# Kernel tuning notes

Hardware: AMD Instinct MI355X
Metric: run time of the kernel (lower is better)

## Reference

```python
import jax, jax.numpy as jnp
import numpy as np

EMBED = 3072
NQ = 32
NKV = 8
HD = EMBED // NQ  # 96
GROUPS = NQ // NKV  # 4
ROPE_BASE = 10000.0


def apply_rope(t, positions):
    # t: [b, h, s, d]; positions: [s] int
    d = t.shape[-1]
    inv_freq = 1.0 / (ROPE_BASE ** (jnp.arange(0, d, 2, dtype=jnp.float32) / d))  # [d/2]
    ang = positions.astype(jnp.float32)[:, None] * inv_freq[None, :]  # [s, d/2]
    cos = jnp.cos(ang)[None, None]  # [1,1,s,d/2]
    sin = jnp.sin(ang)[None, None]
    t1, t2 = t[..., : d // 2], t[..., d // 2 :]
    return jnp.concatenate([t1 * cos - t2 * sin, t2 * cos + t1 * sin], axis=-1)


def setup_inputs() -> dict:
    key = jax.random.key(0)
    k1, k2, k3 = jax.random.split(key, 3)
    b, s = 2, 2048
    x = jax.random.normal(k1, (b, s, EMBED), dtype=jnp.float32)
    positions = jnp.arange(s, dtype=jnp.int32)
    mask = jnp.triu(jnp.ones((s, s), dtype=bool), k=1)  # True = masked (causal)
    qkv_size = NQ * HD + 2 * NKV * HD  # 4608
    W_qkv = jax.random.normal(k2, (qkv_size, EMBED), dtype=jnp.float32) * (EMBED ** -0.5)
    W_o = jax.random.normal(k3, (EMBED, EMBED), dtype=jnp.float32) * (EMBED ** -0.5)
    return {"x": x, "positions": positions, "mask": mask, "W_qkv": W_qkv, "W_o": W_o}


def reference(x, positions, mask, W_qkv, W_o):
    b, s, _ = x.shape
    scaling = HD ** -0.5
    qkv = x @ W_qkv.T  # [b, s, 4608]
    q_size, kv_size = NQ * HD, NKV * HD
    q = qkv[..., :q_size].reshape(b, s, NQ, HD).transpose(0, 2, 1, 3)          # [b,NQ,s,d]
    k = qkv[..., q_size : q_size + kv_size].reshape(b, s, NKV, HD).transpose(0, 2, 1, 3)
    v = qkv[..., q_size + kv_size :].reshape(b, s, NKV, HD).transpose(0, 2, 1, 3)
    q = apply_rope(q, positions)
    k = apply_rope(k, positions)
    q = q.reshape(b, NKV, GROUPS, s, HD)
    scores = jnp.einsum("bkgsd,bktd->bkgst", q, k) * scaling  # [b,NKV,G,s,s]
    scores = jnp.where(mask[None, None, None], -jnp.inf, scores)
    attn = jax.nn.softmax(scores, axis=-1)
    out = jnp.einsum("bkgst,bktd->bkgsd", attn, v)
    out = out.reshape(b, NQ, s, HD).transpose(0, 2, 1, 3).reshape(b, s, NQ * HD)
    return out @ W_o.T
```

## Files before the change

### kernel.cpp

```cpp
#include <hip/hip_runtime.h>
#include <cstdint>

typedef unsigned short u16;
typedef unsigned int u32;
typedef __attribute__((ext_vector_type(4))) float f32x4;
typedef __attribute__((ext_vector_type(8))) __bf16 bf16x8;
typedef __attribute__((ext_vector_type(8))) unsigned short u16x8;
typedef __attribute__((ext_vector_type(4))) unsigned int u32x4;

#define S_LEN 2048
#define BATCH 2
#define NQH 32
#define NKVH 8
#define HD 96
#define EMB 3072
#define QKVN 4608
#define KOFF 3072
#define VOFF 3840
#define KSP 104

__device__ __forceinline__ u16 f2b(float f) {
    u32 u = __float_as_uint(f);
    u32 r = (u + 0x7fffu + ((u >> 16) & 1u)) >> 16;
    return (u16)r;
}
__device__ __forceinline__ float b2f(u16 h) { return __uint_as_float(((u32)h) << 16); }
__device__ __forceinline__ u32 cvtpk(float lo, float hi) {
    u32 r;
    asm("v_cvt_pk_bf16_f32 %0, %1, %2" : "=v"(r) : "v"(lo), "v"(hi));
    return r;
}

__global__ __launch_bounds__(256) void conv_f2b(const float* __restrict__ in,
                                                u16* __restrict__ outp, int n8) {
    const int i = blockIdx.x * 256 + threadIdx.x;
    if (i >= n8) return;
    const f32x4* q = (const f32x4*)(in + (size_t)i * 8);
    const f32x4 a = q[0], b = q[1];
    u16x8 t;
#pragma unroll
    for (int j = 0; j < 4; ++j) {
        t[j] = f2b(a[j]);
        t[j + 4] = f2b(b[j]);
    }
    *(u16x8*)(outp + (size_t)i * 8) = t;
}

typedef __attribute__((address_space(1))) const uint32_t gas_u32;
typedef __attribute__((address_space(3))) uint32_t las_u32;
__device__ __forceinline__ void gld_lds16(const u16* g, u16* l) {
    __builtin_amdgcn_global_load_lds((gas_u32*)g, (las_u32*)l, 16, 0, 0);
}

#define WAITV8 asm volatile("s_waitcnt vmcnt(8)" ::: "memory")
#define LGKM0 asm volatile("s_waitcnt lgkmcnt(0)" ::: "memory")
#define BARRIERM asm volatile("s_barrier" ::: "memory")
#define SCHEDB __builtin_amdgcn_sched_barrier(0)

__device__ __forceinline__ void stage32(const u16* __restrict__ G, int ldg, int k0,
                                        u16* buf, int tid) {
#pragma unroll
    for (int L = 0; L < 2; ++L) {
        const int c = L * 512 + tid;
        const int r = c >> 2;
        const int sg = (c & 3) ^ ((r >> 1) & 3);
        const u16* src = G + (size_t)r * ldg + k0 + sg * 8;
        u16* dst = buf + (L * 512 + (tid & 448)) * 8;
        gld_lds16(src, dst);
    }
}

__device__ __forceinline__ bf16x8 frag32(const u16* buf, int row, int s) {
    const int sg = s ^ ((row >> 1) & 3);
    return *(const bf16x8*)(buf + row * 32 + sg * 8);
}

template <bool OUTF32>
__global__ __launch_bounds__(512, 1) void gemm_bt32(const u16* __restrict__ Ap,
                                                    const u16* __restrict__ Bp,
                                                    void* __restrict__ Cp,
                                                    int M, int N, int K, int ldc) {
    __shared__ __align__(16) u16 S[65536];
    const int tid = threadIdx.x;
    const int lane = tid & 63;
    const int lrow = lane & 15, lhi = lane >> 4;
    const int wid = tid >> 6;
    const int wr = wid >> 2, wc = wid & 3;
    const int bm = blockIdx.y * 256, bn = blockIdx.x * 256;
    const u16* Ab = Ap + (size_t)bm * K;
    const u16* Bb = Bp + (size_t)bn * K;

    f32x4 acc[8][4] = {};
    const int nt = K >> 5;
    const int arow0 = wr * 128 + lrow;
    const int brow0 = wc * 64 + lrow;

#pragma unroll
    for (int t = 0; t < 3; ++t) {
        stage32(Ab, K, t * 32, S + t * 16384, tid);
        stage32(Bb, K, t * 32, S + t * 16384 + 8192, tid);
    }

    for (int t = 0; t < nt; ++t) {
        const u16* Ac = S + (t & 3) * 16384;
        const u16* Bc = Ac + 8192;
        u16* Sn = S + ((t + 3) & 3) * 16384;
        const int kn = (t + 3 < nt) ? (t + 3) * 32 : 0;

        WAITV8;
        BARRIERM;

        bf16x8 af[8], bfr[2];
#pragma unroll
        for (int mi = 0; mi < 8; ++mi) af[mi] = frag32(Ac, arow0 + mi * 16, lhi);
#pragma unroll
        for (int ni = 0; ni < 2; ++ni) bfr[ni] = frag32(Bc, brow0 + ni * 16, lhi);
        stage32(Ab, K, kn, Sn, tid);
        LGKM0;
        SCHEDB;
        __builtin_amdgcn_s_setprio(1);
#pragma unroll
        for (int mi = 0; mi < 8; ++mi)
#pragma unroll
            for (int ni = 0; ni < 2; ++ni)
                acc[mi][ni] = __builtin_amdgcn_mfma_f32_16x16x32_bf16(af[mi], bfr[ni],
                                                                      acc[mi][ni], 0, 0, 0);
        __builtin_amdgcn_s_setprio(0);

#pragma unroll
        for (int ni = 0; ni < 2; ++ni) bfr[ni] = frag32(Bc, brow0 + (ni + 2) * 16, lhi);
        stage32(Bb, K, kn, Sn + 8192, tid);
        LGKM0;
        SCHEDB;
        __builtin_amdgcn_s_setprio(1);
#pragma unroll
        for (int mi = 0; mi < 8; ++mi)
#pragma unroll
            for (int ni = 0; ni < 2; ++ni)
                acc[mi][ni + 2] = __builtin_amdgcn_mfma_f32_16x16x32_bf16(af[mi], bfr[ni],
                                                                          acc[mi][ni + 2], 0, 0, 0);
        __builtin_amdgcn_s_setprio(0);
    }

    const int orow = bm + wr * 128 + lhi * 4;
    const int ocol = bn + wc * 64 + lrow;
#pragma unroll
    for (int mi = 0; mi < 8; ++mi)
#pragma unroll
        for (int ni = 0; ni < 4; ++ni)
#pragma unroll
            for (int r = 0; r < 4; ++r) {
                const size_t idx = (size_t)(orow + mi * 16 + r) * ldc + ocol + ni * 16;
                if constexpr (OUTF32)
                    ((float*)Cp)[idx] = acc[mi][ni][r];
                else
                    ((u16*)Cp)[idx] = f2b(acc[mi][ni][r]);
            }
}

__global__ __launch_bounds__(256) void gqa_rope8(u16* __restrict__ qkv,
                                                 const int* __restrict__ positions) {
    const int i = blockIdx.x * 256 + threadIdx.x;
    const int pc = i % 6;
    int t = i / 6;
    const int head = t % (NQH + NKVH);
    const int bs = t / (NQH + NKVH);
    const int pos = positions[bs & (S_LEN - 1)];
    const size_t base = (size_t)bs * QKVN +
                        (head < NQH ? head * HD : KOFF + (head - NQH) * HD) + pc * 8;
    const u16x8 a = *(const u16x8*)(qkv + base);
    const u16x8 b = *(const u16x8*)(qkv + base + 48);
    u16x8 ra, rb;
#pragma unroll
    for (int jj = 0; jj < 8; ++jj) {
        const int pair = pc * 8 + jj;
        const float invf = __expf(-(float)(2 * pair) * (1.0f / 96.0f) * 9.210340371976184f);
        const float ang = (float)pos * invf;
        float sn, cs;
        __sincosf(ang, &sn, &cs);
        const float t1 = b2f(a[jj]), t2 = b2f(b[jj]);
        ra[jj] = f2b(t1 * cs - t2 * sn);
        rb[jj] = f2b(t2 * cs + t1 * sn);
    }
    *(u16x8*)(qkv + base) = ra;
    *(u16x8*)(qkv + base + 48) = rb;
}

__global__ __launch_bounds__(256) void gqa_attn5(const u16* __restrict__ qkv,
                                                 u16* __restrict__ out) {
    __shared__ __align__(16) u16 Ks[64 * KSP];
    __shared__ __align__(16) u16 Vtmp[64 * 96];
    __shared__ __align__(16) u16 Vt[96 * 72];

    const int tid = threadIdx.x;
    const int wave = tid >> 6, lane = tid & 63;
    const int lrow = lane & 15, lhi = lane >> 4;
    const int bx = blockIdx.x;
    const int qt32 = 63 - (bx >> 4);
    const int kvh = (bx >> 1) & 7, bb = bx & 1;
    const int qh = kvh * 4 + wave;
    const int srow0 = bb * S_LEN + qt32 * 32;
    const int kb_last = (qt32 * 32 + 31) >> 6;
    const float cl2 = 0.10206207261596575f * 1.4426950408889634f;

    bf16x8 bq[2][3];
#pragma unroll
    for (int qt = 0; qt < 2; ++qt)
#pragma unroll
        for (int kd = 0; kd < 3; ++kd)
            bq[qt][kd] = *(const bf16x8*)(qkv + (size_t)(srow0 + qt * 16 + lrow) * QKVN +
                                          qh * 96 + kd * 32 + lhi * 8);

    float m_s[2] = {-3e38f, -3e38f}, l_s[2] = {0.0f, 0.0f};
    f32x4 oacc[6][2] = {};

    const int s0 = lrow + ((lane & 16) ? 32 : 0);
    const int s1 = s0 + 16;
    const bool khi = (lane & 32) != 0;

    const size_t kvrow0 = (size_t)(bb * S_LEN) * QKVN;
    u16x8 kreg[3], vreg[3];

    {
        const size_t kbase = kvrow0 + KOFF + (size_t)kvh * 96;
        const size_t vbase = kvrow0 + VOFF + (size_t)kvh * 96;
#pragma unroll
        for (int i = 0; i < 3; ++i) {
            const int u = tid + 256 * i;
            const int so = (u % 12) * 8, sr = u / 12;
            kreg[i] = *(const u16x8*)(qkv + kbase + (size_t)sr * QKVN + so);
            vreg[i] = *(const u16x8*)(qkv + vbase + (size_t)sr * QKVN + so);
        }
#pragma unroll
        for (int i = 0; i < 3; ++i) {
            const int u = tid + 256 * i;
            const int so = (u % 12) * 8, sr = u / 12;
            *(u16x8*)(Ks + sr * KSP + so) = kreg[i];
            *(u16x8*)(Vtmp + sr * 96 + so) = vreg[i];
        }
        __syncthreads();
#pragma unroll
        for (int i = 0; i < 3; ++i) {
            const int u = tid + 256 * i;
            const int td = u % 96, ts8 = u / 96;
            u16x8 c;
#pragma unroll
            for (int j = 0; j < 8; ++j) c[j] = Vtmp[(ts8 * 8 + j) * 96 + td];
            *(u16x8*)(Vt + td * 72 + ts8 * 8) = c;
        }
    }

    for (int kb = 0; kb <= kb_last; ++kb) {
        if (kb < kb_last) {
            const size_t kbase2 = kvrow0 + (size_t)((kb + 1) * 64) * QKVN + KOFF + kvh * 96;
            const size_t vbase2 = kvrow0 + (size_t)((kb + 1) * 64) * QKVN + VOFF + kvh * 96;
#pragma unroll
            for (int i = 0; i < 3; ++i) {
                const int u = tid + 256 * i;
                const int so = (u % 12) * 8, sr = u / 12;
                kreg[i] = *(const u16x8*)(qkv + kbase2 + (size_t)sr * QKVN + so);
                vreg[i] = *(const u16x8*)(qkv + vbase2 + (size_t)sr * QKVN + so);
            }
        }
        __syncthreads();

        bf16x8 ka[4][3];
#pragma unroll
        for (int kt = 0; kt < 4; ++kt)
#pragma unroll
            for (int kd = 0; kd < 3; ++kd)
                ka[kt][kd] = *(const bf16x8*)(Ks + (kt * 16 + lrow) * KSP + kd * 32 + lhi * 8);

        const int qoff = qt32 * 32 - kb * 64;
        const bool lastkb = (kb == kb_last);
        u32 bp[2][2][4];

#pragma unroll
        for (int qt = 0; qt < 2; ++qt) {
            const int qrelmax = qoff + qt * 16 + 15;
            f32x4 sacc[4] = {};
#pragma unroll
            for (int kt = 0; kt < 4; ++kt) {
                if (lastkb && kt * 16 > qrelmax) continue;
#pragma unroll
                for (int kd = 0; kd < 3; ++kd)
                    sacc[kt] = __builtin_amdgcn_mfma_f32_16x16x32_bf16(ka[kt][kd], bq[qt][kd],
                                                                       sacc[kt], 0, 0, 0);
            }
            float p[4][4];
            float mx = -3e38f;
            if (lastkb) {
                const int qrel = qoff + qt * 16 + lrow;
#pragma unroll
                for (int kt = 0; kt < 4; ++kt)
#pragma unroll
                    for (int r = 0; r < 4; ++r) {
                        const bool live = (kt * 16 + lhi * 4 + r) <= qrel;
                        const float s = live ? sacc[kt][r] : -3e38f;
                        p[kt][r] = s;
                        mx = fmaxf(mx, s);
                    }
            } else {
#pragma unroll
                for (int kt = 0; kt < 4; ++kt)
#pragma unroll
                    for (int r = 0; r < 4; ++r) {
                        p[kt][r] = sacc[kt][r];
                        mx = fmaxf(mx, sacc[kt][r]);
                    }
            }
            mx = fmaxf(mx, __shfl_xor(mx, 16));
            mx = fmaxf(mx, __shfl_xor(mx, 32));
            float mn = m_s[qt];
            if (!__all(mx - mn <= 20.0f)) {
                const float mnew = fmaxf(mn, mx);
                const float alpha = exp2f((mn - mnew) * cl2);
                m_s[qt] = mnew;
                mn = mnew;
                l_s[qt] *= alpha;
#pragma unroll
                for (int dt = 0; dt < 6; ++dt)
#pragma unroll
                    for (int r = 0; r < 4; ++r) oacc[dt][qt][r] *= alpha;
            }
            float rs = 0.0f;
#pragma unroll
            for (int kt = 0; kt < 4; ++kt)
#pragma unroll
                for (int r = 0; r < 4; ++r) {
                    const float pv = exp2f((p[kt][r] - mn) * cl2);
                    p[kt][r] = pv;
                    rs += pv;
                }
            rs += __shfl_xor(rs, 16);
            rs += __shfl_xor(rs, 32);
            l_s[qt] += rs;
            u32 pk[4][2];
#pragma unroll
            for (int kt = 0; kt < 4; ++kt) {
                pk[kt][0] = cvtpk(p[kt][0], p[kt][1]);
                pk[kt][1] = cvtpk(p[kt][2], p[kt][3]);
            }
#pragma unroll
            for (int kk = 0; kk < 2; ++kk) {
                const u32 a0 = (u32)__shfl((int)pk[kk * 2][0], s0, 64);
                const u32 b0 = (u32)__shfl((int)pk[kk * 2 + 1][0], s0, 64);
                const u32 a1 = (u32)__shfl((int)pk[kk * 2][1], s0, 64);
                const u32 b1 = (u32)__shfl((int)pk[kk * 2 + 1][1], s0, 64);
                const u32 a2 = (u32)__shfl((int)pk[kk * 2][0], s1, 64);
                const u32 b2 = (u32)__shfl((int)pk[kk * 2 + 1][0], s1, 64);
                const u32 a3 = (u32)__shfl((int)pk[kk * 2][1], s1, 64);
                const u32 b3 = (u32)__shfl((int)pk[kk * 2 + 1][1], s1, 64);
                bp[qt][kk][0] = khi ? b0 : a0;
                bp[qt][kk][1] = khi ? b1 : a1;
                bp[qt][kk][2] = khi ? b2 : a2;
                bp[qt][kk][3] = khi ? b3 : a3;
            }
        }

#pragma unroll
        for (int dt = 0; dt < 6; ++dt) {
            bf16x8 va[2];
#pragma unroll
            for (int kk = 0; kk < 2; ++kk)
                va[kk] = *(const bf16x8*)(Vt + (dt * 16 + lrow) * 72 + kk * 32 + lhi * 8);
#pragma unroll
            for (int qt = 0; qt < 2; ++qt)
#pragma unroll
                for (int kk = 0; kk < 2; ++kk) {
                    const u32x4 bv = {bp[qt][kk][0], bp[qt][kk][1], bp[qt][kk][2], bp[qt][kk][3]};
                    oacc[dt][qt] = __builtin_amdgcn_mfma_f32_16x16x32_bf16(
                        va[kk], __builtin_bit_cast(bf16x8, bv), oacc[dt][qt], 0, 0, 0);
                }
        }

        __syncthreads();
        if (kb < kb_last) {
#pragma unroll
            for (int i = 0; i < 3; ++i) {
                const int u = tid + 256 * i;
                const int so = (u % 12) * 8, sr = u / 12;
                *(u16x8*)(Ks + sr * KSP + so) = kreg[i];
                *(u16x8*)(Vtmp + sr * 96 + so) = vreg[i];
            }
            __syncthreads();
#pragma unroll
            for (int i = 0; i < 3; ++i) {
                const int u = tid + 256 * i;
                const int td = u % 96, ts8 = u / 96;
                u16x8 c;
#pragma unroll
                for (int j = 0; j < 8; ++j) c[j] = Vtmp[(ts8 * 8 + j) * 96 + td];
                *(u16x8*)(Vt + td * 72 + ts8 * 8) = c;
            }
        }
    }

    const size_t obase = (size_t)srow0 * EMB + qh * 96;
#pragma unroll
    for (int qt = 0; qt < 2; ++qt) {
        const float inv = 1.0f / l_s[qt];
        const size_t rbase = obase + (size_t)(qt * 16 + lrow) * EMB;
#pragma unroll
        for (int dt = 0; dt < 6; ++dt)
#pragma unroll
            for (int rp = 0; rp < 2; ++rp) {
                const u32 pair = cvtpk(oacc[dt][qt][2 * rp] * inv, oacc[dt][qt][2 * rp + 1] * inv);
                *(u32*)(out + rbase + dt * 16 + lhi * 4 + 2 * rp) = pair;
            }
    }
}

extern "C" void kernel_launch(void* const* d_in, const int* in_sizes, int n_in,
                              void* d_out, int out_size, void* d_ws, size_t ws_size,
                              hipStream_t stream) {
    const float* x = (const float*)d_in[0];
    const int* positions = (const int*)d_in[1];
    const float* W_qkv = (const float*)d_in[3];
    const float* W_o = (const float*)d_in[4];
    float* out = (float*)d_out;

    const int M = BATCH * S_LEN;
    const size_t QKV_E = (size_t)M * QKVN;
    const size_t X_E = (size_t)M * EMB;
    const size_t WQKV_E = (size_t)QKVN * EMB;
    const size_t WO_E = (size_t)EMB * EMB;

    u16* qkv = (u16*)d_ws;
    u16* scratch = qkv + QKV_E;
    u16* xb = scratch;
    u16* wqkvb = (u16*)d_out;
    u16* wob = (u16*)d_ws;

    conv_f2b<<<(int)(X_E / 8 / 256), 256, 0, stream>>>(x, xb, (int)(X_E / 8));
    conv_f2b<<<(int)(WQKV_E / 8 / 256), 256, 0, stream>>>(W_qkv, wqkvb, (int)(WQKV_E / 8));
    gemm_bt32<false>
        <<<dim3(QKVN / 256, M / 256), 512, 0, stream>>>(xb, wqkvb, qkv, M, QKVN, EMB, QKVN);
    gqa_rope8<<<(BATCH * S_LEN * (NQH + NKVH) * 6) / 256, 256, 0, stream>>>(qkv, positions);
    gqa_attn5<<<dim3(1024), 256, 0, stream>>>(qkv, scratch);
    conv_f2b<<<(int)(WO_E / 8 / 256), 256, 0, stream>>>(W_o, wob, (int)(WO_E / 8));
    gemm_bt32<true>
        <<<dim3(EMB / 256, M / 256), 512, 0, stream>>>(scratch, wob, out, M, EMB, EMB, EMB);
}
```

Before: 597.3 us.

## Split longest causal attention tiles across two blocks with merge kernel

The 512 query tiles with the most keys (the last quarter of rows per batch) are now split into two blocks. Each block processes half of the key range and writes unnormalized fp32 partial outputs plus its max and sum into d_out as scratch. A new merge kernel combines the two halves with log-sum-exp rescaling and writes bf16. This is meant to reduce tail imbalance in the causal attention grid, at the cost of an extra launch and fp32 partial traffic.

```diff
diff --git a/kernel.cpp b/kernel.cpp
--- a/kernel.cpp
+++ b/kernel.cpp
@@ -18,6 +18,7 @@
 #define KOFF 3072
 #define VOFF 3840
 #define KSP 104
+#define CL2 0.14724601498759837f
 
 __device__ __forceinline__ u16 f2b(float f) {
     u32 u = __float_as_uint(f);
@@ -186,8 +187,9 @@
     *(u16x8*)(qkv + base + 48) = rb;
 }
 
-__global__ __launch_bounds__(256) void gqa_attn5(const u16* __restrict__ qkv,
-                                                 u16* __restrict__ out) {
+__global__ __launch_bounds__(256) void gqa_attn6(const u16* __restrict__ qkv,
+                                                 u16* __restrict__ out,
+                                                 float* __restrict__ part) {
     __shared__ __align__(16) u16 Ks[64 * KSP];
     __shared__ __align__(16) u16 Vtmp[64 * 96];
     __shared__ __align__(16) u16 Vt[96 * 72];
@@ -196,12 +198,33 @@
     const int wave = tid >> 6, lane = tid & 63;
     const int lrow = lane & 15, lhi = lane >> 4;
     const int bx = blockIdx.x;
-    const int qt32 = 63 - (bx >> 4);
-    const int kvh = (bx >> 1) & 7, bb = bx & 1;
+
+    int qt32, kvh, bb, sp, kb_lo, kb_hi;
+    bool dosplit;
+    if (bx < 768) {
+        qt32 = 47 - (bx >> 4);
+        kvh = (bx >> 1) & 7;
+        bb = bx & 1;
+        sp = 0;
+        kb_lo = 0;
+        kb_hi = (qt32 * 32 + 31) >> 6;
+        dosplit = false;
+    } else {
+        const int s = bx - 768;
+        qt32 = 63 - (s >> 5);
+        const int r = s & 31;
+        kvh = (r >> 2) & 7;
+        bb = (r >> 1) & 1;
+        sp = r & 1;
+        const int kb_last = (qt32 * 32 + 31) >> 6;
+        const int half = (kb_last + 1) >> 1;
+        kb_lo = sp ? half : 0;
+        kb_hi = sp ? kb_last : half - 1;
+        dosplit = true;
+    }
+    const int kb_abs_last = (qt32 * 32 + 31) >> 6;
     const int qh = kvh * 4 + wave;
     const int srow0 = bb * S_LEN + qt32 * 32;
-    const int kb_last = (qt32 * 32 + 31) >> 6;
-    const float cl2 = 0.10206207261596575f * 1.4426950408889634f;
 
     bf16x8 bq[2][3];
 #pragma unroll
@@ -222,8 +245,8 @@
     u16x8 kreg[3], vreg[3];
 
     {
-        const size_t kbase = kvrow0 + KOFF + (size_t)kvh * 96;
-        const size_t vbase = kvrow0 + VOFF + (size_t)kvh * 96;
+        const size_t kbase = kvrow0 + (size_t)(kb_lo * 64) * QKVN + KOFF + (size_t)kvh * 96;
+        const size_t vbase = kvrow0 + (size_t)(kb_lo * 64) * QKVN + VOFF + (size_t)kvh * 96;
 #pragma unroll
         for (int i = 0; i < 3; ++i) {
             const int u = tid + 256 * i;
@@ -250,8 +273,8 @@
         }
     }
 
-    for (int kb = 0; kb <= kb_last; ++kb) {
-        if (kb < kb_last) {
+    for (int kb = kb_lo; kb <= kb_hi; ++kb) {
+        if (kb < kb_hi) {
             const size_t kbase2 = kvrow0 + (size_t)((kb + 1) * 64) * QKVN + KOFF + kvh * 96;
             const size_t vbase2 = kvrow0 + (size_t)((kb + 1) * 64) * QKVN + VOFF + kvh * 96;
 #pragma unroll
@@ -272,7 +295,7 @@
                 ka[kt][kd] = *(const bf16x8*)(Ks + (kt * 16 + lrow) * KSP + kd * 32 + lhi * 8);
 
         const int qoff = qt32 * 32 - kb * 64;
-        const bool lastkb = (kb == kb_last);
+        const bool lastkb = (kb == kb_abs_last);
         u32 bp[2][2][4];
 
 #pragma unroll
@@ -314,7 +337,7 @@
             float mn = m_s[qt];
             if (!__all(mx - mn <= 20.0f)) {
                 const float mnew = fmaxf(mn, mx);
-                const float alpha = exp2f((mn - mnew) * cl2);
+                const float alpha = exp2f((mn - mnew) * CL2);
                 m_s[qt] = mnew;
                 mn = mnew;
                 l_s[qt] *= alpha;
@@ -328,7 +351,7 @@
             for (int kt = 0; kt < 4; ++kt)
 #pragma unroll
                 for (int r = 0; r < 4; ++r) {
-                    const float pv = exp2f((p[kt][r] - mn) * cl2);
+                    const float pv = exp2f((p[kt][r] - mn) * CL2);
                     p[kt][r] = pv;
                     rs += pv;
                 }
@@ -375,7 +398,7 @@
         }
 
         __syncthreads();
-        if (kb < kb_last) {
+        if (kb < kb_hi) {
 #pragma unroll
             for (int i = 0; i < 3; ++i) {
                 const int u = tid + 256 * i;
@@ -396,19 +419,71 @@
         }
     }
 
-    const size_t obase = (size_t)srow0 * EMB + qh * 96;
-#pragma unroll
-    for (int qt = 0; qt < 2; ++qt) {
-        const float inv = 1.0f / l_s[qt];
-        const size_t rbase = obase + (size_t)(qt * 16 + lrow) * EMB;
-#pragma unroll
-        for (int dt = 0; dt < 6; ++dt)
-#pragma unroll
-            for (int rp = 0; rp < 2; ++rp) {
-                const u32 pair = cvtpk(oacc[dt][qt][2 * rp] * inv, oacc[dt][qt][2 * rp + 1] * inv);
-                *(u32*)(out + rbase + dt * 16 + lhi * 4 + 2 * rp) = pair;
-            }
-    }
+    if (!dosplit) {
+        const size_t obase = (size_t)srow0 * EMB + qh * 96;
+#pragma unroll
+        for (int qt = 0; qt < 2; ++qt) {
+            const float inv = 1.0f / l_s[qt];
+            const size_t rbase = obase + (size_t)(qt * 16 + lrow) * EMB;
+#pragma unroll
+            for (int dt = 0; dt < 6; ++dt)
+#pragma unroll
+                for (int rp = 0; rp < 2; ++rp) {
+                    const u32 pair =
+                        cvtpk(oacc[dt][qt][2 * rp] * inv, oacc[dt][qt][2 * rp + 1] * inv);
+                    *(u32*)(out + rbase + dt * 16 + lhi * 4 + 2 * rp) = pair;
+                }
+        }
+    } else {
+        float* opart = part + (size_t)sp * 1024 * EMB;
+        float* ml = part + (size_t)2 * 1024 * EMB;
+        const int prow_b = bb * 512 + (qt32 - 48) * 32;
+#pragma unroll
+        for (int qt = 0; qt < 2; ++qt) {
+            const int prow = prow_b + qt * 16 + lrow;
+            float* rb = opart + (size_t)prow * EMB + qh * 96;
+#pragma unroll
+            for (int dt = 0; dt < 6; ++dt)
+                *(f32x4*)(rb + dt * 16 + lhi * 4) = oacc[dt][qt];
+            if (lhi == 0) {
+                float* mlp = ml + ((size_t)(sp * 1024 + prow) * 32 + qh) * 2;
+                mlp[0] = m_s[qt];
+                mlp[1] = l_s[qt];
+            }
+        }
+    }
+}
+
+__global__ __launch_bounds__(256) void attn_merge(const float* __restrict__ part,
+                                                  u16* __restrict__ out) {
+    const int j = blockIdx.x * 256 + threadIdx.x;
+    const int oct = j % 12;
+    const int t = j / 12;
+    const int qh = t & 31;
+    const int prow = t >> 5;
+    const float* ml = part + (size_t)2 * 1024 * EMB;
+    const float* m0p = ml + ((size_t)prow * 32 + qh) * 2;
+    const float* m1p = ml + ((size_t)(1024 + prow) * 32 + qh) * 2;
+    const float m0 = m0p[0], l0 = m0p[1], m1 = m1p[0], l1 = m1p[1];
+    const float M = fmaxf(m0, m1);
+    const float e0 = exp2f((m0 - M) * CL2);
+    const float e1 = exp2f((m1 - M) * CL2);
+    const float inv = 1.0f / (e0 * l0 + e1 * l1);
+    const float* o0 = part + (size_t)prow * EMB + qh * 96 + oct * 8;
+    const float* o1 = o0 + (size_t)1024 * EMB;
+    const int bb = prow >> 9;
+    const int qt32 = 48 + ((prow & 511) >> 5);
+    const int qrow = prow & 31;
+    const int srow = bb * S_LEN + qt32 * 32 + qrow;
+    u16* dst = out + (size_t)srow * EMB + qh * 96 + oct * 8;
+    u32 w[4];
+#pragma unroll
+    for (int pr = 0; pr < 4; ++pr) {
+        const float a = (e0 * o0[2 * pr] + e1 * o1[2 * pr]) * inv;
+        const float b = (e0 * o0[2 * pr + 1] + e1 * o1[2 * pr + 1]) * inv;
+        w[pr] = cvtpk(a, b);
+    }
+    *(u32x4*)dst = {w[0], w[1], w[2], w[3]};
 }
 
 extern "C" void kernel_launch(void* const* d_in, const int* in_sizes, int n_in,
@@ -430,6 +505,7 @@
     u16* scratch = qkv + QKV_E;
     u16* xb = scratch;
     u16* wqkvb = (u16*)d_out;
+    float* part = (float*)d_out;
     u16* wob = (u16*)d_ws;
 
     conv_f2b<<<(int)(X_E / 8 / 256), 256, 0, stream>>>(x, xb, (int)(X_E / 8));
@@ -437,7 +513,8 @@
     gemm_bt32<false>
         <<<dim3(QKVN / 256, M / 256), 512, 0, stream>>>(xb, wqkvb, qkv, M, QKVN, EMB, QKVN);
     gqa_rope8<<<(BATCH * S_LEN * (NQH + NKVH) * 6) / 256, 256, 0, stream>>>(qkv, positions);
-    gqa_attn5<<<dim3(1024), 256, 0, stream>>>(qkv, scratch);
+    gqa_attn6<<<dim3(1280), 256, 0, stream>>>(qkv, scratch, part);
+    attn_merge<<<dim3(1536), 256, 0, stream>>>(part, scratch);
     conv_f2b<<<(int)(WO_E / 8 / 256), 256, 0, stream>>>(W_o, wob, (int)(WO_E / 8));
     gemm_bt32<true>
         <<<dim3(EMB / 256, M / 256), 512, 0, stream>>>(scratch, wob, out, M, EMB, EMB, EMB);
```

Result: slower. 629.3 us (+5.4%).
